# Optimization experiments

Measured on AMD Instinct MI355X. Metric: run time of the kernel, lower is better.

The kernel has to match this reference:

```python
import jax, jax.numpy as jnp
import numpy as np
import math

BN_EPS = 1e-5
L2_EPS = 1e-12
TEMPARATURE = 0.01
Q_IN_DIM = 256


def _masked_bn(y, mask, gamma, beta):
    # y: [S, L, D], mask: [S, L] float (1 = valid packed row).
    # Emulates BatchNorm1d (training mode) over the packed valid rows.
    m = mask[..., None]
    cnt = jnp.sum(mask)
    mean = jnp.sum(y * m, axis=(0, 1)) / cnt
    var = jnp.sum(jnp.square(y - mean) * m, axis=(0, 1)) / cnt  # biased var
    return (y - mean) * jax.lax.rsqrt(var + BN_EPS) * gamma + beta


def _ctx_proj(x, W, b, gamma, beta, mask, normalize):
    y = jnp.einsum('sld,od->slo', x, W) + b
    y = jax.nn.relu(_masked_bn(y, mask, gamma, beta))
    if normalize:
        n = jnp.linalg.norm(y, axis=-1, keepdims=True)
        y = y / jnp.maximum(n, L2_EPS)
    return y


def setup_inputs() -> dict:
    key = jax.random.key(0)
    ks = jax.random.split(key, 8)
    S, La, Lb = 256, 128, 512
    Dq, Dkv, Dqk, Dv = 256, 265, 512, 512
    A = jax.random.normal(ks[0], (S, La, Dq), jnp.float32)
    B = jax.random.normal(ks[1], (S, Lb, Dkv), jnp.float32)
    a_lens = jax.random.randint(ks[2], (S,), 1, La + 1, jnp.int32)
    b_lens = jax.random.randint(ks[3], (S,), 1, Lb + 1, jnp.int32)
    pk = jax.random.split(ks[4], 4)
    sc = 0.05
    return {
        'A': A, 'B': B, 'a_lens': a_lens, 'b_lens': b_lens,
        'Wq': sc * jax.random.normal(pk[0], (Dqk, Dq), jnp.float32),
        'bq': jnp.zeros((Dqk,), jnp.float32),
        'gq': jnp.ones((Dqk,), jnp.float32),
        'betaq': jnp.zeros((Dqk,), jnp.float32),
        'Wk': sc * jax.random.normal(pk[1], (Dqk, Dkv), jnp.float32),
        'bk': jnp.zeros((Dqk,), jnp.float32),
        'gk': jnp.ones((Dqk,), jnp.float32),
        'betak': jnp.zeros((Dqk,), jnp.float32),
        'Wv': sc * jax.random.normal(pk[2], (Dv, Dkv), jnp.float32),
        'bv': jnp.zeros((Dv,), jnp.float32),
        'gv': jnp.ones((Dv,), jnp.float32),
        'betav': jnp.zeros((Dv,), jnp.float32),
        'Wf': sc * jax.random.normal(pk[3], (Dq, Dv), jnp.float32),
        'bf': jnp.zeros((Dq,), jnp.float32),
        'gf': jnp.ones((Dq,), jnp.float32),
        'betaf': jnp.zeros((Dq,), jnp.float32),
    }


def reference(A, B, a_lens, b_lens,
              Wq, bq, gq, betaq,
              Wk, bk, gk, betak,
              Wv, bv, gv, betav,
              Wf, bf, gf, betaf):
    S, La, _ = A.shape
    Lb = B.shape[1]
    mask_a = (jnp.arange(La)[None, :] < a_lens[:, None]).astype(A.dtype)  # [S, La]
    mask_b = (jnp.arange(Lb)[None, :] < b_lens[:, None]).astype(B.dtype)  # [S, Lb]

    q = _ctx_proj(A, Wq, bq, gq, betaq, mask_a, True)   # [S, La, Dqk]
    k = _ctx_proj(B, Wk, bk, gk, betak, mask_b, True)   # [S, Lb, Dqk]
    v = _ctx_proj(B, Wv, bv, gv, betav, mask_b, True)   # [S, Lb, Dv]

    scaler = 1.0 / (TEMPARATURE * math.sqrt(Q_IN_DIM))
    scores = jnp.einsum('sad,sbd->sab', q, k) * scaler  # [S, La, Lb]
    scores = jnp.where(mask_b[:, None, :] > 0, scores, -1e30)
    w = jax.nn.softmax(scores, axis=-1)
    wv = jnp.einsum('sab,sbd->sad', w, v)               # [S, La, Dv]

    f = _ctx_proj(wv, Wf, bf, gf, betaf, mask_a, False)  # [S, La, Dq]
    return f * mask_a[..., None]
```

## Files before the change

kernel.cpp:

```cpp
#include <hip/hip_runtime.h>
#include <hip/hip_bf16.h>
#include <stdint.h>


typedef __attribute__((ext_vector_type(8))) short short8;
typedef __attribute__((ext_vector_type(4))) float floatx4;

__device__ __forceinline__ float bf2f(short h) {
    union { unsigned u; float f; } c;
    c.u = ((unsigned)(unsigned short)h) << 16;
    return c.f;
}
__device__ __forceinline__ short f2bf(float f) {
    union { float f; unsigned u; } c;
    c.f = f;
    unsigned u = c.u + 0x7fffu + ((c.u >> 16) & 1u);
    return (short)(u >> 16);
}

__device__ __forceinline__ void async_cp16(const short* g, short* l) {
    __builtin_amdgcn_global_load_lds(
        (const __attribute__((address_space(1))) unsigned int*)g,
        (__attribute__((address_space(3))) unsigned int*)l, 16, 0, 0);
}

__device__ __forceinline__ short8 cvt8load(const float* p) {
    float4 f0 = *(const float4*)(p);
    float4 f1 = *(const float4*)(p + 4);
    short8 r;
    r[0] = f2bf(f0.x); r[1] = f2bf(f0.y); r[2] = f2bf(f0.z); r[3] = f2bf(f0.w);
    r[4] = f2bf(f1.x); r[5] = f2bf(f1.y); r[6] = f2bf(f1.z); r[7] = f2bf(f1.w);
    return r;
}
__device__ __forceinline__ short8 cvt8guard(const float* row, int c0, int Kin) {
    short8 r;
#pragma unroll
    for (int j = 0; j < 8; j++) {
        int c = c0 + j;
        r[j] = (c < Kin) ? f2bf(row[c]) : (short)0;
    }
    return r;
}

__global__ __launch_bounds__(256) void cvt_pad(const float* __restrict__ in,
                                               short* __restrict__ out,
                                               int kin, int kout) {
    long row = blockIdx.x;
    const float* src = in + row * (long)kin;
    short* dst = out + row * (long)kout;
    for (int c = threadIdx.x; c < kout; c += 256)
        dst[c] = (c < kin) ? f2bf(src[c]) : (short)0;
}

__global__ __launch_bounds__(256, 3)
void gemm128(const short* __restrict__ X,
             const short* __restrict__ W0, const short* __restrict__ W1,
             const float* __restrict__ bias0, const float* __restrict__ bias1,
             short* __restrict__ Y0, short* __restrict__ Y1,
             float* __restrict__ st0, float* __restrict__ st1,
             int N, int Kp, const int* __restrict__ lens, int Lshift,
             int nShift, int dual)
{
    __shared__ short SH[24576];
    const int lin = blockIdx.x;
    const int xcd = lin & 7, sl = lin >> 3;
    const int nb = sl & ((1 << nShift) - 1);
    const int ms = sl >> nShift;
    const int m0 = (ms * 8 + xcd) * 128;
    int g = 0, n0;
    if (dual) { g = nb & 1; n0 = (nb >> 1) * 128; } else { n0 = nb * 128; }
    const short* W    = g ? W1 : W0;
    const float* bias = g ? bias1 : bias0;
    short* Y          = g ? Y1 : Y0;
    float* stats      = g ? st1 : st0;

    const int tid = threadIdx.x;
    const int l = tid & 63, w = tid >> 6;
    const int quad = l >> 4, l15 = l & 15;
    const int wr = w & 1, wc = w >> 1;
    const int mo = wr * 64, no = wc * 64;

    floatx4 acc[4][4];
#pragma unroll
    for (int i = 0; i < 4; i++)
#pragma unroll
        for (int j = 0; j < 4; j++) acc[i][j] = (floatx4){0.f, 0.f, 0.f, 0.f};

    const int srow = tid >> 2;
    const int scol = (tid & 3) * 8;
    const short* Xs = X + (long)(m0 + srow) * Kp + scol;
    const short* Ws = W + (long)(n0 + srow) * Kp + scol;
    const long strideR = (long)64 * Kp;
    const int nsteps = Kp >> 5;

    auto stage = [&](int buf, int t) {
        short* At = SH + buf * 8192;
        short* Bt = At + 4096;
        const short* Xk = Xs + t * 32;
        const short* Wk = Ws + t * 32;
        async_cp16(Xk,           At + tid * 8);
        async_cp16(Xk + strideR, At + 2048 + tid * 8);
        async_cp16(Wk,           Bt + tid * 8);
        async_cp16(Wk + strideR, Bt + 2048 + tid * 8);
    };

    stage(0, 0);
    if (nsteps > 1) stage(1, 1);
    if (nsteps > 2) stage(2, 2);

    int cur = 0;
    for (int t = 0; t < nsteps; t++) {
        if (t + 2 < nsteps)      asm volatile("s_waitcnt vmcnt(8)" ::: "memory");
        else if (t + 1 < nsteps) asm volatile("s_waitcnt vmcnt(4)" ::: "memory");
        else                     asm volatile("s_waitcnt vmcnt(0)" ::: "memory");
        __builtin_amdgcn_s_barrier();
        __builtin_amdgcn_sched_barrier(0);

        const short* At = SH + cur * 8192;
        const short* Bt = At + 4096;
        short8 af[4], bfr[4];
#pragma unroll
        for (int i = 0; i < 4; i++)
            af[i] = *(const short8*)(At + (mo + i * 16 + l15) * 32 + quad * 8);
#pragma unroll
        for (int j = 0; j < 4; j++)
            bfr[j] = *(const short8*)(Bt + (no + j * 16 + l15) * 32 + quad * 8);
#pragma unroll
        for (int i = 0; i < 4; i++)
#pragma unroll
            for (int j = 0; j < 4; j++)
                acc[i][j] = __builtin_amdgcn_mfma_f32_16x16x32_bf16(af[i], bfr[j], acc[i][j], 0, 0, 0);

        __builtin_amdgcn_sched_barrier(0);
        __builtin_amdgcn_s_barrier();
        if (t + 3 < nsteps) stage(cur, t + 3);
        cur = (cur == 2) ? 0 : cur + 1;
    }

    const int Lmask = (1 << Lshift) - 1;
    float msk[4][4];
#pragma unroll
    for (int i = 0; i < 4; i++)
#pragma unroll
        for (int r = 0; r < 4; r++) {
            int rg = m0 + mo + i * 16 + quad * 4 + r;
            msk[i][r] = ((rg & Lmask) < lens[rg >> Lshift]) ? 1.f : 0.f;
        }
    float bv[4];
#pragma unroll
    for (int j = 0; j < 4; j++) bv[j] = bias[n0 + no + j * 16 + l15];

#pragma unroll
    for (int j = 0; j < 4; j++) {
        float ps = 0.f, pss = 0.f;
#pragma unroll
        for (int i = 0; i < 4; i++)
#pragma unroll
            for (int r = 0; r < 4; r++) {
                float v = acc[i][j][r] + bv[j];
                ps += v * msk[i][r];
                pss += v * v * msk[i][r];
            }
        ps  += __shfl_xor(ps, 16, 64);  ps  += __shfl_xor(ps, 32, 64);
        pss += __shfl_xor(pss, 16, 64); pss += __shfl_xor(pss, 32, 64);
        if (l < 16) {
            atomicAdd(&stats[n0 + no + j * 16 + l15], ps);
            atomicAdd(&stats[N + n0 + no + j * 16 + l15], pss);
        }
    }

    short* Cs = SH;
#pragma unroll
    for (int pass = 0; pass < 2; pass++) {
        __syncthreads();
        if (wr == pass) {
#pragma unroll
            for (int j = 0; j < 4; j++)
#pragma unroll
                for (int i = 0; i < 4; i++)
#pragma unroll
                    for (int r = 0; r < 4; r++)
                        Cs[(i * 16 + quad * 4 + r) * 132 + no + j * 16 + l15] =
                            f2bf(acc[i][j][r] + bv[j]);
        }
        __syncthreads();
#pragma unroll
        for (int c = 0; c < 4; c++) {
            int e = c * 2048 + tid * 8;
            int row = e >> 7, col = e & 127;
            short8 vv = *(const short8*)(Cs + row * 132 + col);
            *(short8*)(Y + (long)(m0 + pass * 64 + row) * N + n0 + col) = vv;
        }
    }
}

template<bool XBF16, bool KAL>
__global__ __launch_bounds__(256, 2)
void gemm_bt(const void* __restrict__ Xp, const float* __restrict__ W,
             const float* __restrict__ bias, short* __restrict__ Y,
             int N, int Kin, int Kp, float* __restrict__ stats,
             const int* __restrict__ lens, int Lshift)
{
    __shared__ short At[128 * 32];
    __shared__ short Bt[128 * 32];
    const int m0 = blockIdx.x * 128;
    const int n0 = blockIdx.y * 128;
    const int tid = threadIdx.x;
    const int w = tid >> 6, l = tid & 63;
    const int quad = l >> 4, l15 = l & 15;
    const int mo = (w & 1) * 64, no = (w >> 1) * 64;

    floatx4 acc[4][4];
#pragma unroll
    for (int i = 0; i < 4; i++)
#pragma unroll
        for (int j = 0; j < 4; j++) acc[i][j] = (floatx4){0.f, 0.f, 0.f, 0.f};

    const int srow = tid >> 2;
    const int sc8 = (tid & 3) * 8;

    for (int k0 = 0; k0 < Kp; k0 += 32) {
        __syncthreads();
        const int c0 = k0 + sc8;
        short8 a0, a1, b0, b1;
        if (XBF16) {
            const short* X = (const short*)Xp;
            a0 = *(const short8*)(X + (long)(m0 + srow) * Kp + c0);
            a1 = *(const short8*)(X + (long)(m0 + 64 + srow) * Kp + c0);
        } else {
            const float* X = (const float*)Xp;
            if (KAL) {
                a0 = cvt8load(X + (long)(m0 + srow) * Kin + c0);
                a1 = cvt8load(X + (long)(m0 + 64 + srow) * Kin + c0);
            } else {
                a0 = cvt8guard(X + (long)(m0 + srow) * Kin, c0, Kin);
                a1 = cvt8guard(X + (long)(m0 + 64 + srow) * Kin, c0, Kin);
            }
        }
        if (KAL) {
            b0 = cvt8load(W + (long)(n0 + srow) * Kin + c0);
            b1 = cvt8load(W + (long)(n0 + 64 + srow) * Kin + c0);
        } else {
            b0 = cvt8guard(W + (long)(n0 + srow) * Kin, c0, Kin);
            b1 = cvt8guard(W + (long)(n0 + 64 + srow) * Kin, c0, Kin);
        }
        *(short8*)(At + srow * 32 + sc8) = a0;
        *(short8*)(At + (64 + srow) * 32 + sc8) = a1;
        *(short8*)(Bt + srow * 32 + sc8) = b0;
        *(short8*)(Bt + (64 + srow) * 32 + sc8) = b1;
        __syncthreads();
        short8 af[4], bfr[4];
#pragma unroll
        for (int i = 0; i < 4; i++) {
            af[i]  = *(const short8*)(At + (mo + i * 16 + l15) * 32 + quad * 8);
            bfr[i] = *(const short8*)(Bt + (no + i * 16 + l15) * 32 + quad * 8);
        }
#pragma unroll
        for (int i = 0; i < 4; i++)
#pragma unroll
            for (int j = 0; j < 4; j++)
                acc[i][j] = __builtin_amdgcn_mfma_f32_16x16x32_bf16(af[i], bfr[j], acc[i][j], 0, 0, 0);
    }

    const int Lmask = (1 << Lshift) - 1;
    float msk[4][4];
#pragma unroll
    for (int i = 0; i < 4; i++)
#pragma unroll
        for (int r = 0; r < 4; r++) {
            int rg = m0 + mo + i * 16 + quad * 4 + r;
            msk[i][r] = ((rg & Lmask) < lens[rg >> Lshift]) ? 1.f : 0.f;
        }
#pragma unroll
    for (int j = 0; j < 4; j++) {
        int colj = n0 + no + j * 16 + l15;
        float bvs = bias[colj];
        float ps = 0.f, pss = 0.f;
#pragma unroll
        for (int i = 0; i < 4; i++)
#pragma unroll
            for (int r = 0; r < 4; r++) {
                int rg = m0 + mo + i * 16 + quad * 4 + r;
                float v = acc[i][j][r] + bvs;
                Y[(long)rg * N + colj] = f2bf(v);
                ps += v * msk[i][r];
                pss += v * v * msk[i][r];
            }
        ps  += __shfl_xor(ps, 16, 64);  ps  += __shfl_xor(ps, 32, 64);
        pss += __shfl_xor(pss, 16, 64); pss += __shfl_xor(pss, 32, 64);
        if (l < 16) {
            atomicAdd(&stats[colj], ps);
            atomicAdd(&stats[N + colj], pss);
        }
    }
}

__global__ void finalize_stats(float* __restrict__ stats, const float* __restrict__ g,
                               const float* __restrict__ beta,
                               const int* __restrict__ lens, int C)
{
    __shared__ int lred[256];
    int t = threadIdx.x;
    if (t < 256) lred[t] = lens[t];
    __syncthreads();
    for (int s2 = 128; s2 > 0; s2 >>= 1) {
        if (t < s2) lred[t] += lred[t + s2];
        __syncthreads();
    }
    float cnt = (float)lred[0];
    if (t < C) {
        float mean = stats[t] / cnt;
        float var = fmaxf(stats[C + t] / cnt - mean * mean, 0.f);
        float a = rsqrtf(var + 1e-5f) * g[t];
        stats[t] = a;
        stats[C + t] = beta[t] - mean * a;
    }
}

__global__ __launch_bounds__(256)
void apply_norm512(short* __restrict__ Y, const float* __restrict__ stats)
{
    int w = threadIdx.x >> 6, l = threadIdx.x & 63;
    long row = (long)blockIdx.x * 4 + w;
    short8 yv = *(const short8*)(Y + row * 512 + l * 8);
    float v[8];
    float ss = 0.f;
#pragma unroll
    for (int i = 0; i < 8; i++) {
        int c = l * 8 + i;
        float t = fmaxf(bf2f(yv[i]) * stats[c] + stats[512 + c], 0.f);
        v[i] = t;
        ss += t * t;
    }
#pragma unroll
    for (int off = 1; off < 64; off <<= 1) ss += __shfl_xor(ss, off, 64);
    float scl = 1.f / fmaxf(sqrtf(ss), 1e-12f);
    short8 o;
#pragma unroll
    for (int i = 0; i < 8; i++) o[i] = f2bf(v[i] * scl);
    *(short8*)(Y + row * 512 + l * 8) = o;
}

__global__ __launch_bounds__(256)
void attention(const short* __restrict__ q, const short* __restrict__ k,
               const short* __restrict__ v, const int* __restrict__ b_lens,
               short* __restrict__ wv, int wvStride)
{
    __shared__ short tile[32 * 520];
    __shared__ short Pscr[4][16 * 40];
    const int lin = blockIdx.x;
    const int xcd = lin & 7, sl = lin >> 3;
    const int a0 = (sl & 1) * 64;
    const int s = (sl >> 1) * 8 + xcd;
    const int tid = threadIdx.x;
    const int w = tid >> 6, l = tid & 63;
    const int quad = l >> 4, l15 = l & 15;
    const int blen = b_lens[s];
    const int sr = tid >> 3;
    const int scg = (tid & 7) * 8;

    short8 qf[16];
    const short* qbase = q + ((long)(s * 128 + a0 + w * 16 + l15)) * 512 + quad * 8;
#pragma unroll
    for (int kk = 0; kk < 16; kk++) qf[kk] = *(const short8*)(qbase + kk * 32);

    floatx4 sc[32];
#pragma unroll
    for (int i = 0; i < 32; i++) sc[i] = (floatx4){0.f, 0.f, 0.f, 0.f};

    const short* kbase = k + (long)s * 512 * 512;
    for (int bt2 = 0; bt2 < 16; ++bt2) {
        __syncthreads();
        const short* krow = kbase + (long)(bt2 * 32 + sr) * 512;
#pragma unroll
        for (int i = 0; i < 2; i++) {
            short8 t0 = *(const short8*)(krow + i * 256 + scg);
            short8 t1 = *(const short8*)(krow + i * 256 + 64 + scg);
            short8 t2 = *(const short8*)(krow + i * 256 + 128 + scg);
            short8 t3 = *(const short8*)(krow + i * 256 + 192 + scg);
            *(short8*)(&tile[sr * 520 + i * 256 + scg]) = t0;
            *(short8*)(&tile[sr * 520 + i * 256 + 64 + scg]) = t1;
            *(short8*)(&tile[sr * 520 + i * 256 + 128 + scg]) = t2;
            *(short8*)(&tile[sr * 520 + i * 256 + 192 + scg]) = t3;
        }
        __syncthreads();
#pragma unroll
        for (int kk = 0; kk < 16; kk++) {
            short8 f0 = *(const short8*)(&tile[l15 * 520 + kk * 32 + quad * 8]);
            short8 f1 = *(const short8*)(&tile[(16 + l15) * 520 + kk * 32 + quad * 8]);
            sc[bt2 * 2]     = __builtin_amdgcn_mfma_f32_16x16x32_bf16(qf[kk], f0, sc[bt2 * 2], 0, 0, 0);
            sc[bt2 * 2 + 1] = __builtin_amdgcn_mfma_f32_16x16x32_bf16(qf[kk], f1, sc[bt2 * 2 + 1], 0, 0, 0);
        }
    }

    const float scaler = 6.25f;
    float mrow[4] = {-__builtin_inff(), -__builtin_inff(), -__builtin_inff(), -__builtin_inff()};
#pragma unroll
    for (int bt = 0; bt < 32; ++bt) {
        bool valid = (bt * 16 + l15) < blen;
#pragma unroll
        for (int r = 0; r < 4; r++) {
            float v2 = valid ? sc[bt][r] * scaler : -__builtin_inff();
            sc[bt][r] = v2;
            mrow[r] = fmaxf(mrow[r], v2);
        }
    }
#pragma unroll
    for (int r = 0; r < 4; r++) {
#pragma unroll
        for (int off = 1; off < 16; off <<= 1)
            mrow[r] = fmaxf(mrow[r], __shfl_xor(mrow[r], off, 64));
    }
    float ssum[4] = {0.f, 0.f, 0.f, 0.f};
#pragma unroll
    for (int bt = 0; bt < 32; ++bt)
#pragma unroll
        for (int r = 0; r < 4; r++) {
            float p = __expf(sc[bt][r] - mrow[r]);
            sc[bt][r] = p;
            ssum[r] += p;
        }
#pragma unroll
    for (int r = 0; r < 4; r++) {
#pragma unroll
        for (int off = 1; off < 16; off <<= 1) ssum[r] += __shfl_xor(ssum[r], off, 64);
        ssum[r] = 1.f / ssum[r];
    }

    short8 pf[16];
    short* Pw = Pscr[w];
#pragma unroll
    for (int kk = 0; kk < 16; kk++) {
#pragma unroll
        for (int half = 0; half < 2; half++)
#pragma unroll
            for (int r = 0; r < 4; r++)
                Pw[(quad * 4 + r) * 40 + half * 16 + l15] = f2bf(sc[kk * 2 + half][r] * ssum[r]);
        pf[kk] = *(const short8*)(&Pw[l15 * 40 + quad * 8]);
    }

    const short* vbase = v + (long)s * 512 * 512;
    short* wvbase = wv + (long)(s * 128 + a0 + w * 16 + quad * 4) * wvStride;
    for (int dt = 0; dt < 16; ++dt) {
        __syncthreads();
#pragma unroll
        for (int round = 0; round < 2; round++) {
            int b = round * 256 + tid;
            const short* vr = vbase + (long)b * 512 + dt * 32;
            short8 x0 = *(const short8*)(vr);
            short8 x1 = *(const short8*)(vr + 8);
            short8 x2 = *(const short8*)(vr + 16);
            short8 x3 = *(const short8*)(vr + 24);
#pragma unroll
            for (int j = 0; j < 8; j++) {
                tile[j * 520 + b]        = x0[j];
                tile[(8 + j) * 520 + b]  = x1[j];
                tile[(16 + j) * 520 + b] = x2[j];
                tile[(24 + j) * 520 + b] = x3[j];
            }
        }
        __syncthreads();
        floatx4 o0 = (floatx4){0.f, 0.f, 0.f, 0.f};
        floatx4 o1 = (floatx4){0.f, 0.f, 0.f, 0.f};
#pragma unroll
        for (int kk = 0; kk < 16; kk++) {
            short8 f0 = *(const short8*)(&tile[l15 * 520 + kk * 32 + quad * 8]);
            short8 f1 = *(const short8*)(&tile[(16 + l15) * 520 + kk * 32 + quad * 8]);
            o0 = __builtin_amdgcn_mfma_f32_16x16x32_bf16(pf[kk], f0, o0, 0, 0, 0);
            o1 = __builtin_amdgcn_mfma_f32_16x16x32_bf16(pf[kk], f1, o1, 0, 0, 0);
        }
#pragma unroll
        for (int r = 0; r < 4; r++) {
            wvbase[(long)r * wvStride + dt * 32 + l15]      = f2bf(o0[r]);
            wvbase[(long)r * wvStride + dt * 32 + 16 + l15] = f2bf(o1[r]);
        }
    }

    if (wvStride > 512) {
        int r = tid >> 2, cb = (tid & 3) * 16;
        short8 z = (short8){0, 0, 0, 0, 0, 0, 0, 0};
        short* pz = wv + (long)(s * 128 + a0 + r) * wvStride + 512 + cb;
        *(short8*)(pz) = z;
        *(short8*)(pz + 8) = z;
    }
}

__global__ __launch_bounds__(256)
void apply_f(const short* __restrict__ Yf, const float* __restrict__ stats,
             const int* __restrict__ a_lens, float* __restrict__ out)
{
    const long total = (long)32768 * 256;
    for (long e = (long)blockIdx.x * 256 + threadIdx.x; e < total; e += (long)gridDim.x * 256) {
        int c = (int)(e & 255);
        long row = e >> 8;
        int sI = (int)(row >> 7), pos = (int)(row & 127);
        float v = fmaxf(bf2f(Yf[e]) * stats[c] + stats[256 + c], 0.f);
        out[e] = (pos < a_lens[sI]) ? v : 0.f;
    }
}

extern "C" void kernel_launch(void* const* d_in, const int* in_sizes, int n_in,
                              void* d_out, int out_size, void* d_ws, size_t ws_size,
                              hipStream_t stream)
{
    (void)in_sizes; (void)n_in; (void)out_size;
    const float* A     = (const float*)d_in[0];
    const float* B     = (const float*)d_in[1];
    const int* a_lens  = (const int*)d_in[2];
    const int* b_lens  = (const int*)d_in[3];
    const float* Wq    = (const float*)d_in[4];
    const float* bq    = (const float*)d_in[5];
    const float* gq    = (const float*)d_in[6];
    const float* betaq = (const float*)d_in[7];
    const float* Wk    = (const float*)d_in[8];
    const float* bk    = (const float*)d_in[9];
    const float* gk    = (const float*)d_in[10];
    const float* betak = (const float*)d_in[11];
    const float* Wv    = (const float*)d_in[12];
    const float* bv    = (const float*)d_in[13];
    const float* gv    = (const float*)d_in[14];
    const float* betav = (const float*)d_in[15];
    const float* Wf    = (const float*)d_in[16];
    const float* bfp   = (const float*)d_in[17];
    const float* gf    = (const float*)d_in[18];
    const float* betaf = (const float*)d_in[19];
    float* out = (float*)d_out;
    char* base = (char*)d_ws;

    const size_t oWqb = 0;
    const size_t oWkb = oWqb + 294912;
    const size_t oWvb = oWkb + 294912;
    const size_t oWfb = oWvb + 294912;
    const size_t oBbf = oWfb + 294912;
    const size_t oQb  = oBbf + 75497472;
    const size_t oYv  = oQb + 33554432;
    const size_t oKb  = oYv + 134217728;
    const size_t oSt  = oKb + 134217728;
    const size_t FAST_NEED = oSt + 16384;

    if (ws_size >= FAST_NEED) {
        short* Wqb = (short*)(base + oWqb);
        short* Wkb = (short*)(base + oWkb);
        short* Wvb = (short*)(base + oWvb);
        short* Wfb = (short*)(base + oWfb);
        short* Bbf = (short*)(base + oBbf);
        short* qb  = (short*)(base + oQb);
        short* Yv  = (short*)(base + oYv);
        short* kb  = (short*)(base + oKb);
        short* Abf = (short*)(base + oKb);
        short* wvb = (short*)(base + oBbf);
        short* Yf  = (short*)(base + oQb);
        float* stQ = (float*)(base + oSt);
        float* stK = stQ + 1024;
        float* stV = stQ + 2048;
        float* stF = stQ + 3072;

        hipMemsetAsync(stQ, 0, 16384, stream);

        cvt_pad<<<32768, 256, 0, stream>>>(A, Abf, 256, 288);
        cvt_pad<<<131072, 256, 0, stream>>>(B, Bbf, 265, 288);
        cvt_pad<<<512, 256, 0, stream>>>(Wq, Wqb, 256, 288);
        cvt_pad<<<512, 256, 0, stream>>>(Wk, Wkb, 265, 288);
        cvt_pad<<<512, 256, 0, stream>>>(Wv, Wvb, 265, 288);
        cvt_pad<<<256, 256, 0, stream>>>(Wf, Wfb, 512, 576);

        gemm128<<<1024, 256, 0, stream>>>(
            Abf, Wqb, Wqb, bq, bq, qb, qb, stQ, stQ, 512, 288, a_lens, 7, 2, 0);
        gemm128<<<8192, 256, 0, stream>>>(
            Bbf, Wvb, Wkb, bv, bk, Yv, kb, stV, stK, 512, 288, b_lens, 9, 3, 1);

        finalize_stats<<<1, 512, 0, stream>>>(stV, gv, betav, b_lens, 512);
        finalize_stats<<<1, 512, 0, stream>>>(stK, gk, betak, b_lens, 512);
        finalize_stats<<<1, 512, 0, stream>>>(stQ, gq, betaq, a_lens, 512);
        apply_norm512<<<32768, 256, 0, stream>>>(Yv, stV);
        apply_norm512<<<32768, 256, 0, stream>>>(kb, stK);
        apply_norm512<<<8192, 256, 0, stream>>>(qb, stQ);

        attention<<<512, 256, 0, stream>>>(qb, kb, Yv, b_lens, wvb, 576);

        gemm128<<<512, 256, 0, stream>>>(
            wvb, Wfb, Wfb, bfp, bfp, Yf, Yf, stF, stF, 256, 576, a_lens, 7, 1, 0);
        finalize_stats<<<1, 512, 0, stream>>>(stF, gf, betaf, a_lens, 256);
        apply_f<<<8192, 256, 0, stream>>>(Yf, stF, a_lens, out);
        return;
    }

    short* qb  = (short*)(base);
    short* Yv  = (short*)(base + 33554432);
    short* kb  = (short*)(base + 33554432 + 134217728);
    short* wvb = (short*)(base + 33554432 + 2L * 134217728);
    float* stQ = (float*)(base + 2L * 33554432 + 2L * 134217728);
    float* stK = stQ + 1024;
    float* stV = stQ + 2048;
    float* stF = stQ + 3072;
    short* Yf  = qb;

    hipMemsetAsync(stQ, 0, 16384, stream);

    gemm_bt<false, true><<<dim3(256, 4), 256, 0, stream>>>(
        A, Wq, bq, qb, 512, 256, 256, stQ, a_lens, 7);
    gemm_bt<false, false><<<dim3(1024, 4), 256, 0, stream>>>(
        B, Wv, bv, Yv, 512, 265, 288, stV, b_lens, 9);
    finalize_stats<<<1, 512, 0, stream>>>(stV, gv, betav, b_lens, 512);
    apply_norm512<<<32768, 256, 0, stream>>>(Yv, stV);
    gemm_bt<false, false><<<dim3(1024, 4), 256, 0, stream>>>(
        B, Wk, bk, kb, 512, 265, 288, stK, b_lens, 9);
    finalize_stats<<<1, 512, 0, stream>>>(stK, gk, betak, b_lens, 512);
    apply_norm512<<<32768, 256, 0, stream>>>(kb, stK);
    finalize_stats<<<1, 512, 0, stream>>>(stQ, gq, betaq, a_lens, 512);
    apply_norm512<<<8192, 256, 0, stream>>>(qb, stQ);
    attention<<<512, 256, 0, stream>>>(qb, kb, Yv, b_lens, wvb, 512);
    gemm_bt<true, true><<<dim3(256, 2), 256, 0, stream>>>(
        wvb, Wf, bfp, Yf, 256, 512, 512, stF, a_lens, 7);
    finalize_stats<<<1, 512, 0, stream>>>(stF, gf, betaf, a_lens, 256);
    apply_f<<<8192, 256, 0, stream>>>(Yf, stF, a_lens, out);
}
```

Measured before the change: 837.2 us.

## Compute K and V projections in one block sharing the B tile

Adds a gemm128x2 kernel in which each block loads one 128-row tile of B and computes both the V and K projections against two weight tiles, keeping two accumulator sets. The activation tile is therefore read from global memory once rather than once per projection, and the launch has half as many blocks. It uses a 3-stage async pipeline and a larger shared-memory buffer, and lowers the occupancy hint to 2 blocks per CU. The two accumulator sets raise register pressure, which may reduce latency hiding.

After: 837.5 us. About the same (+0.0%).

```diff
diff --git a/kernel.cpp b/kernel.cpp
--- a/kernel.cpp
+++ b/kernel.cpp
@@ -50,6 +50,186 @@
     short* dst = out + row * (long)kout;
     for (int c = threadIdx.x; c < kout; c += 256)
         dst[c] = (c < kin) ? f2bf(src[c]) : (short)0;
+}
+
+__global__ __launch_bounds__(256, 2)
+void gemm128x2(const short* __restrict__ X,
+               const short* __restrict__ W0, const short* __restrict__ W1,
+               const float* __restrict__ bias0, const float* __restrict__ bias1,
+               short* __restrict__ Y0, short* __restrict__ Y1,
+               float* __restrict__ st0, float* __restrict__ st1,
+               int N, int Kp, const int* __restrict__ lens, int Lshift,
+               int nShift)
+{
+    __shared__ short SH[36864];
+    const int lin = blockIdx.x;
+    const int xcd = lin & 7, sl = lin >> 3;
+    const int nb = sl & ((1 << nShift) - 1);
+    const int ms = sl >> nShift;
+    const int m0 = (ms * 8 + xcd) * 128;
+    const int n0 = nb * 128;
+
+    const int tid = threadIdx.x;
+    const int l = tid & 63, w = tid >> 6;
+    const int quad = l >> 4, l15 = l & 15;
+    const int wr = w & 1, wc = w >> 1;
+    const int mo = wr * 64, no = wc * 64;
+
+    floatx4 acc0[4][4], acc1[4][4];
+#pragma unroll
+    for (int i = 0; i < 4; i++)
+#pragma unroll
+        for (int j = 0; j < 4; j++) {
+            acc0[i][j] = (floatx4){0.f, 0.f, 0.f, 0.f};
+            acc1[i][j] = (floatx4){0.f, 0.f, 0.f, 0.f};
+        }
+
+    int srow[2], scolS[2];
+#pragma unroll
+    for (int c = 0; c < 2; c++) {
+        int L = tid * 16 + c * 4096;
+        int S = L ^ ((((L >> 6) ^ (L >> 8)) & 1) << 4)
+                  ^ (((L >> 7) & 1) << 5)
+                  ^ (((L >> 8) & 1) << 6);
+        srow[c] = S >> 6;
+        scolS[c] = (S & 48) >> 1;
+    }
+    const short* Xs[2];
+    const short* W0s[2];
+    const short* W1s[2];
+#pragma unroll
+    for (int c = 0; c < 2; c++) {
+        Xs[c]  = X  + (long)(m0 + srow[c]) * Kp + scolS[c];
+        W0s[c] = W0 + (long)(n0 + srow[c]) * Kp + scolS[c];
+        W1s[c] = W1 + (long)(n0 + srow[c]) * Kp + scolS[c];
+    }
+    const int nsteps = Kp >> 5;
+
+    int rsA[4], rsB[4];
+#pragma unroll
+    for (int i = 0; i < 4; i++) {
+        int rA = mo + i * 16 + l15;
+        int rB = no + i * 16 + l15;
+        rsA[i] = (rA << 6) ^ ((rA & 7) << 4) ^ (quad << 4);
+        rsB[i] = (rB << 6) ^ ((rB & 7) << 4) ^ (quad << 4);
+    }
+
+    auto stage = [&](int buf, int t) {
+        short* At = SH + buf * 12288;
+        short* B0t = At + 4096;
+        short* B1t = At + 8192;
+        const int ko = t * 32;
+#pragma unroll
+        for (int c = 0; c < 2; c++)
+            async_cp16(Xs[c] + ko, At + c * 2048 + tid * 8);
+#pragma unroll
+        for (int c = 0; c < 2; c++)
+            async_cp16(W0s[c] + ko, B0t + c * 2048 + tid * 8);
+#pragma unroll
+        for (int c = 0; c < 2; c++)
+            async_cp16(W1s[c] + ko, B1t + c * 2048 + tid * 8);
+    };
+
+    stage(0, 0);
+    if (nsteps > 1) stage(1, 1);
+    if (nsteps > 2) stage(2, 2);
+
+    int cur = 0;
+    for (int t = 0; t < nsteps; t++) {
+        if (t + 2 < nsteps)      asm volatile("s_waitcnt vmcnt(12)" ::: "memory");
+        else if (t + 1 < nsteps) asm volatile("s_waitcnt vmcnt(6)" ::: "memory");
+        else                     asm volatile("s_waitcnt vmcnt(0)" ::: "memory");
+        __builtin_amdgcn_s_barrier();
+        __builtin_amdgcn_sched_barrier(0);
+
+        const char* At = (const char*)(SH + cur * 12288);
+        const char* B0t = At + 8192;
+        const char* B1t = At + 16384;
+        short8 af[4], bfr[4];
+#pragma unroll
+        for (int i = 0; i < 4; i++)
+            af[i] = *(const short8*)(At + rsA[i]);
+#pragma unroll
+        for (int j = 0; j < 4; j++)
+            bfr[j] = *(const short8*)(B0t + rsB[j]);
+#pragma unroll
+        for (int i = 0; i < 4; i++)
+#pragma unroll
+            for (int j = 0; j < 4; j++)
+                acc0[i][j] = __builtin_amdgcn_mfma_f32_16x16x32_bf16(af[i], bfr[j], acc0[i][j], 0, 0, 0);
+#pragma unroll
+        for (int j = 0; j < 4; j++)
+            bfr[j] = *(const short8*)(B1t + rsB[j]);
+#pragma unroll
+        for (int i = 0; i < 4; i++)
+#pragma unroll
+            for (int j = 0; j < 4; j++)
+                acc1[i][j] = __builtin_amdgcn_mfma_f32_16x16x32_bf16(af[i], bfr[j], acc1[i][j], 0, 0, 0);
+
+        __builtin_amdgcn_sched_barrier(0);
+        __builtin_amdgcn_s_barrier();
+        if (t + 3 < nsteps) stage(cur, t + 3);
+        cur = (cur == 2) ? 0 : cur + 1;
+    }
+
+    const int Lmask = (1 << Lshift) - 1;
+    float msk[4][4];
+#pragma unroll
+    for (int i = 0; i < 4; i++)
+#pragma unroll
+        for (int r = 0; r < 4; r++) {
+            int rg = m0 + mo + i * 16 + quad * 4 + r;
+            msk[i][r] = ((rg & Lmask) < lens[rg >> Lshift]) ? 1.f : 0.f;
+        }
+    short* Cs = SH;
+
+    auto epi = [&](floatx4 (&acc)[4][4], const float* bias, float* stats, short* Y) {
+        float bv[4];
+#pragma unroll
+        for (int j = 0; j < 4; j++) bv[j] = bias[n0 + no + j * 16 + l15];
+#pragma unroll
+        for (int j = 0; j < 4; j++) {
+            float ps = 0.f, pss = 0.f;
+#pragma unroll
+            for (int i = 0; i < 4; i++)
+#pragma unroll
+                for (int r = 0; r < 4; r++) {
+                    float v = acc[i][j][r] + bv[j];
+                    ps += v * msk[i][r];
+                    pss += v * v * msk[i][r];
+                }
+            ps  += __shfl_xor(ps, 16, 64);  ps  += __shfl_xor(ps, 32, 64);
+            pss += __shfl_xor(pss, 16, 64); pss += __shfl_xor(pss, 32, 64);
+            if (l < 16) {
+                atomicAdd(&stats[n0 + no + j * 16 + l15], ps);
+                atomicAdd(&stats[N + n0 + no + j * 16 + l15], pss);
+            }
+        }
+#pragma unroll
+        for (int pass = 0; pass < 2; pass++) {
+            __syncthreads();
+            if (wr == pass) {
+#pragma unroll
+                for (int j = 0; j < 4; j++)
+#pragma unroll
+                    for (int i = 0; i < 4; i++)
+#pragma unroll
+                        for (int r = 0; r < 4; r++)
+                            Cs[(i * 16 + quad * 4 + r) * 132 + no + j * 16 + l15] =
+                                f2bf(acc[i][j][r] + bv[j]);
+            }
+            __syncthreads();
+#pragma unroll
+            for (int c = 0; c < 4; c++) {
+                int e = c * 2048 + tid * 8;
+                int row = e >> 7, col = e & 127;
+                short8 vv = *(const short8*)(Cs + row * 132 + col);
+                *(short8*)(Y + (long)(m0 + pass * 64 + row) * N + n0 + col) = vv;
+            }
+        }
+    };
+    epi(acc0, bias0, st0, Y0);
+    epi(acc1, bias1, st1, Y1);
 }
 
 __global__ __launch_bounds__(256, 3)
@@ -566,8 +746,8 @@
 
         gemm128<<<1024, 256, 0, stream>>>(
             Abf, Wqb, Wqb, bq, bq, qb, qb, stQ, stQ, 512, 288, a_lens, 7, 2, 0);
-        gemm128<<<8192, 256, 0, stream>>>(
-            Bbf, Wvb, Wkb, bv, bk, Yv, kb, stV, stK, 512, 288, b_lens, 9, 3, 1);
+        gemm128x2<<<4096, 256, 0, stream>>>(
+            Bbf, Wvb, Wkb, bv, bk, Yv, kb, stV, stK, 512, 288, b_lens, 9, 2);
 
         finalize_stats<<<1, 512, 0, stream>>>(stV, gv, betav, b_lens, 512);
         finalize_stats<<<1, 512, 0, stream>>>(stK, gk, betak, b_lens, 512);
```
